# Optimization experiments

Hardware: AMD Instinct MI355X
Metric: run time of the kernel (lower is better)

## Reference

```python
import jax, jax.numpy as jnp
import numpy as np

B, L, E, H = 1, 4096, 1024, 16
D = E // H
EPS = 1e-6


def setup_inputs() -> dict:
    key = jax.random.key(0)
    k1, k2, k3 = jax.random.split(key, 3)
    # fan-in scaled init to keep activations sane
    x = jax.random.normal(k1, (B, L, E), dtype=jnp.float32)
    qkv_w = jax.random.normal(k2, (E, 3 * E), dtype=jnp.float32) / np.sqrt(E)
    qkv_b = jnp.zeros((3 * E,), dtype=jnp.float32)
    out_w = jax.random.normal(k3, (E, E), dtype=jnp.float32) / np.sqrt(E)
    out_b = jnp.zeros((E,), dtype=jnp.float32)
    return {"x": x, "qkv_w": qkv_w, "qkv_b": qkv_b, "out_w": out_w, "out_b": out_b}


def reference(x, qkv_w, qkv_b, out_w, out_b):
    b, l, e = x.shape
    qkv = x @ qkv_w + qkv_b                      # (B, L, 3E)
    q, k, v = jnp.split(qkv, 3, axis=-1)
    # (B, L, E) -> (B, H, L, D)
    q = q.reshape(b, l, H, D).transpose(0, 2, 1, 3)
    k = k.reshape(b, l, H, D).transpose(0, 2, 1, 3)
    v = v.reshape(b, l, H, D).transpose(0, 2, 1, 3)
    q_prime = jax.nn.elu(q) + 1.0
    k_prime = jax.nn.elu(k) + 1.0
    # cumulative sum of per-position outer products k'_l v_l^T : (B,H,L,D,D)
    kv_prod = jnp.einsum('bhld,bhle->bhlde', k_prime, v)
    kv_cumsum = jnp.cumsum(kv_prod, axis=2)
    context = jnp.einsum('bhld,bhlde->bhle', q_prime, kv_cumsum)  # (B,H,L,D)
    k_cumsum = jnp.cumsum(k_prime, axis=2)                        # (B,H,L,D)
    norm = jnp.einsum('bhld,bhld->bhl', q_prime, k_cumsum)        # (B,H,L)
    output = context / (norm[..., None] + EPS)
    output = output.transpose(0, 2, 1, 3).reshape(b, l, e)
    return output @ out_w + out_b
```

## Files before the change

kernel.cpp:

```cpp
#include <hip/hip_runtime.h>
#include <cstddef>
#include <cstdint>

#define L_SEQ 4096
#define EMB   1024
#define NH    16
#define HD    64
#define N3    3072
#define CHUNK 64
#define NCHUNK 64
#define EPS 1e-6f

typedef __attribute__((ext_vector_type(8))) short   bf16x8;
typedef __attribute__((ext_vector_type(4))) short   bf16x4;
typedef __attribute__((ext_vector_type(4))) float   floatx4;

#define AS1 __attribute__((address_space(1)))
#define AS3 __attribute__((address_space(3)))

__device__ __forceinline__ void gload_lds16(const void* g, void* l) {
    __builtin_amdgcn_global_load_lds((AS1 const unsigned int*)g,
                                     (AS3 unsigned int*)l, 16, 0, 0);
}

__device__ __forceinline__ short f2bf(float f) {
    union { float f; unsigned u; } a; a.f = f;
    unsigned r = a.u + 0x7fffu + ((a.u >> 16) & 1u);
    return (short)(r >> 16);
}
__device__ __forceinline__ float bf2f(short s) {
    union { unsigned u; float f; } a; a.u = ((unsigned)(unsigned short)s) << 16;
    return a.f;
}

__device__ __forceinline__ void transpose_tile(const float* __restrict__ W,
                                               short* __restrict__ WT,
                                               int K, int N, int bx, int by,
                                               float (*t)[65], int tid)
{
    const int r  = tid >> 4;
    const int c4 = (tid & 15) << 2;
#pragma unroll
    for (int s = 0; s < 4; ++s) {
        const int k = r + s * 16;
        const floatx4 v = *(const floatx4*)&W[(size_t)(by * 64 + k) * N + bx * 64 + c4];
        t[k][c4 + 0] = v[0]; t[k][c4 + 1] = v[1];
        t[k][c4 + 2] = v[2]; t[k][c4 + 3] = v[3];
    }
    __syncthreads();
#pragma unroll
    for (int s = 0; s < 4; ++s) {
        const int n = r + s * 16;
        bf16x4 o;
        o[0] = f2bf(t[c4 + 0][n]); o[1] = f2bf(t[c4 + 1][n]);
        o[2] = f2bf(t[c4 + 2][n]); o[3] = f2bf(t[c4 + 3][n]);
        *(bf16x4*)&WT[(size_t)(bx * 64 + n) * K + by * 64 + c4] = o;
    }
}

__global__ __launch_bounds__(256)
void prep(const float* __restrict__ x, short* __restrict__ xb,
          const float* __restrict__ qkv_w, short* __restrict__ qwt,
          const float* __restrict__ out_w, short* __restrict__ owt)
{
    __shared__ float t[64][65];
    const int b = blockIdx.x;
    const int tid = threadIdx.x;
    if (b < 2048) {
        const int i = b * 256 + tid;
        const floatx4 a = *(const floatx4*)(x + (size_t)i * 8);
        const floatx4 c = *(const floatx4*)(x + (size_t)i * 8 + 4);
        bf16x8 o;
        o[0] = f2bf(a[0]); o[1] = f2bf(a[1]); o[2] = f2bf(a[2]); o[3] = f2bf(a[3]);
        o[4] = f2bf(c[0]); o[5] = f2bf(c[1]); o[6] = f2bf(c[2]); o[7] = f2bf(c[3]);
        *(bf16x8*)(xb + (size_t)i * 8) = o;
    } else if (b < 2048 + 768) {
        const int u = b - 2048;
        transpose_tile(qkv_w, qwt, EMB, N3, u % 48, u / 48, t, tid);
    } else {
        const int u = b - 2816;
        transpose_tile(out_w, owt, EMB, EMB, u & 15, u >> 4, t, tid);
    }
}

#define CST 136

__global__ __launch_bounds__(256)
void mfma_gemm_qkv(const short* __restrict__ A, const short* __restrict__ BT,
                   const float* __restrict__ bias,
                   short* __restrict__ OQ, short* __restrict__ OK,
                   short* __restrict__ OV, int N, int K)
{
    __shared__ __align__(16) short smem[128 * CST];
    short* pan[4] = { smem, smem + 4096, smem + 8192, smem + 12288 };
    const int tid  = threadIdx.x;
    const int lane = tid & 63;
    const int wave = tid >> 6;
    const int wm = (wave >> 1) * 64;
    const int wn = (wave & 1) * 64;
    const int bx = blockIdx.x;
    const int by = blockIdx.y;
    const int frow = lane & 15;
    const int quad = lane >> 4;
    const int fko  = quad << 3;

    const short* Ab = A  + (size_t)(by * 128) * K;
    const short* Bb = BT + (size_t)(bx * 128) * K;

    floatx4 acc[4][4] = {};

    for (int k0 = 0; k0 < K; k0 += 64) {
#pragma unroll
        for (int p = 0; p < 2; ++p) {
            const int kp = k0 + p * 32;
#pragma unroll
            for (int q = 0; q < 2; ++q) {
                const int ia = q * 256 + tid;
                const int row = ia >> 2;
                const int kc  = (ia & 3) << 3;
                gload_lds16(Ab + (size_t)row * K + kp + kc, &pan[p * 2 + 0][ia << 3]);
                gload_lds16(Bb + (size_t)row * K + kp + kc, &pan[p * 2 + 1][ia << 3]);
            }
        }
        __syncthreads();
#pragma unroll
        for (int p = 0; p < 2; ++p) {
            bf16x8 af[4], bfv[4];
#pragma unroll
            for (int mi = 0; mi < 4; ++mi)
                af[mi] = *(const bf16x8*)&pan[p * 2 + 0][(wm + mi * 16 + frow) * 32 + fko];
#pragma unroll
            for (int ni = 0; ni < 4; ++ni)
                bfv[ni] = *(const bf16x8*)&pan[p * 2 + 1][(wn + ni * 16 + frow) * 32 + fko];
#pragma unroll
            for (int mi = 0; mi < 4; ++mi)
#pragma unroll
                for (int ni = 0; ni < 4; ++ni)
                    acc[mi][ni] = __builtin_amdgcn_mfma_f32_16x16x32_bf16(
                        af[mi], bfv[ni], acc[mi][ni], 0, 0, 0);
        }
        __syncthreads();
    }

    const int rq = quad << 2;
#pragma unroll
    for (int ni = 0; ni < 4; ++ni) {
        const int n = bx * 128 + wn + ni * 16 + frow;
        const float bv = bias[n];
        const bool do_elu = (n >> 10) < 2;
#pragma unroll
        for (int mi = 0; mi < 4; ++mi)
#pragma unroll
            for (int r = 0; r < 4; ++r) {
                float v = acc[mi][ni][r] + bv;
                if (do_elu) v = (v > 0.f) ? (v + 1.f) : __expf(v);
                smem[(wm + mi * 16 + rq + r) * CST + wn + ni * 16 + frow] = f2bf(v);
            }
    }
    __syncthreads();
#pragma unroll
    for (int t = 0; t < 8; ++t) {
        const int idx = t * 256 + tid;
        const int mm = idx >> 4;
        const int c8 = (idx & 15) << 3;
        const bf16x8 val = *(const bf16x8*)&smem[mm * CST + c8];
        const int n0 = bx * 128 + c8;
        const int rsel = n0 >> 10;
        const int h  = (n0 & 1023) >> 6;
        const int d  = n0 & 63;
        short* base = (rsel == 0) ? OQ : (rsel == 1 ? OK : OV);
        *(bf16x8*)&base[((size_t)(h * L_SEQ + by * 128 + mm)) * HD + d] = val;
    }
}

__global__ __launch_bounds__(256)
void mfma_gemm_out(const short* __restrict__ A, const short* __restrict__ BT,
                   const float* __restrict__ bias, float* __restrict__ OF,
                   int N, int K)
{
    __shared__ __align__(16) short smem[12288];
    short* pan[4] = { smem, smem + 2048, smem + 6144, smem + 8192 };
    const int tid  = threadIdx.x;
    const int lane = tid & 63;
    const int wave = tid >> 6;
    const int wm = (wave >> 1) * 32;
    const int wn = (wave & 1) * 64;
    const int bx = blockIdx.x;
    const int by = blockIdx.y;
    const int frow = lane & 15;
    const int quad = lane >> 4;
    const int fko  = quad << 3;

    const short* Ab = A  + (size_t)(by * 64) * K;
    const short* Bb = BT + (size_t)(bx * 128) * K;

    floatx4 acc[2][4] = {};

    for (int k0 = 0; k0 < K; k0 += 64) {
#pragma unroll
        for (int p = 0; p < 2; ++p) {
            const int kp = k0 + p * 32;
            {
                const int row = tid >> 2;
                const int kc  = (tid & 3) << 3;
                gload_lds16(Ab + (size_t)row * K + kp + kc, &pan[p * 2 + 0][tid << 3]);
            }
#pragma unroll
            for (int q = 0; q < 2; ++q) {
                const int ib = q * 256 + tid;
                const int row = ib >> 2;
                const int kc  = (ib & 3) << 3;
                gload_lds16(Bb + (size_t)row * K + kp + kc, &pan[p * 2 + 1][ib << 3]);
            }
        }
        __syncthreads();
#pragma unroll
        for (int p = 0; p < 2; ++p) {
            bf16x8 af[2], bfv[4];
#pragma unroll
            for (int mi = 0; mi < 2; ++mi)
                af[mi] = *(const bf16x8*)&pan[p * 2 + 0][(wm + mi * 16 + frow) * 32 + fko];
#pragma unroll
            for (int ni = 0; ni < 4; ++ni)
                bfv[ni] = *(const bf16x8*)&pan[p * 2 + 1][(wn + ni * 16 + frow) * 32 + fko];
#pragma unroll
            for (int mi = 0; mi < 2; ++mi)
#pragma unroll
                for (int ni = 0; ni < 4; ++ni)
                    acc[mi][ni] = __builtin_amdgcn_mfma_f32_16x16x32_bf16(
                        af[mi], bfv[ni], acc[mi][ni], 0, 0, 0);
        }
        __syncthreads();
    }

    const int rq = quad << 2;
#pragma unroll
    for (int ni = 0; ni < 4; ++ni) {
        const int n = bx * 128 + wn + ni * 16 + frow;
        const float bv = bias[n];
#pragma unroll
        for (int mi = 0; mi < 2; ++mi)
#pragma unroll
            for (int r = 0; r < 4; ++r) {
                const int m = by * 64 + wm + mi * 16 + rq + r;
                OF[(size_t)m * N + n] = acc[mi][ni][r] + bv;
            }
    }
}

#define SP 72

__global__ __launch_bounds__(256, 4)
void chunk_state(const short* __restrict__ Kb, const short* __restrict__ Vb,
                 short* __restrict__ ScTb, float* __restrict__ zc)
{
    __shared__ __align__(16) short Vt[64 * SP];
    __shared__ __align__(16) short Kt[64 * SP];
    const int c = blockIdx.x, h = blockIdx.y;
    const int tid = threadIdx.x, lane = tid & 63, wave = tid >> 6;
    const int frow = lane & 15;
    const int quad = lane >> 4;
    const int fko  = quad << 3;
    const int wm   = wave << 4;
    const short* Kg = Kb + ((size_t)h * L_SEQ + (size_t)c * CHUNK) * HD;
    const short* Vg = Vb + ((size_t)h * L_SEQ + (size_t)c * CHUNK) * HD;

#pragma unroll
    for (int q = 0; q < 2; ++q) {
        const int idx = q * 256 + tid;
        const int l = idx >> 3, c8 = (idx & 7) << 3;
        const bf16x8 vv = *(const bf16x8*)&Vg[l * 64 + c8];
        const bf16x8 kk = *(const bf16x8*)&Kg[l * 64 + c8];
#pragma unroll
        for (int j = 0; j < 8; ++j) {
            Vt[(c8 + j) * SP + l] = vv[j];
            Kt[(c8 + j) * SP + l] = kk[j];
        }
    }
    __syncthreads();

    const bf16x8 af0 = *(const bf16x8*)&Vt[(wm + frow) * SP + fko];
    const bf16x8 af1 = *(const bf16x8*)&Vt[(wm + frow) * SP + 32 + fko];

    floatx4 acc[4] = {};
#pragma unroll
    for (int n = 0; n < 4; ++n) {
        const bf16x8 kf0 = *(const bf16x8*)&Kt[(n * 16 + frow) * SP + fko];
        const bf16x8 kf1 = *(const bf16x8*)&Kt[(n * 16 + frow) * SP + 32 + fko];
        acc[n] = __builtin_amdgcn_mfma_f32_16x16x32_bf16(af0, kf0, acc[n], 0, 0, 0);
        acc[n] = __builtin_amdgcn_mfma_f32_16x16x32_bf16(af1, kf1, acc[n], 0, 0, 0);
    }

    short* Sout = ScTb + (size_t)(h * NCHUNK + c) * 4096;
#pragma unroll
    for (int n = 0; n < 4; ++n)
#pragma unroll
        for (int r = 0; r < 4; ++r) {
            const int e = wm + quad * 4 + r;
            const int d = n * 16 + frow;
            Sout[e * 64 + d] = f2bf(acc[n][r]);
        }

    if (wave == 0) {
        bf16x8 ones;
#pragma unroll
        for (int j = 0; j < 8; ++j) ones[j] = (short)0x3F80;
        floatx4 zacc[4] = {};
#pragma unroll
        for (int n = 0; n < 4; ++n) {
            const bf16x8 kf0 = *(const bf16x8*)&Kt[(n * 16 + frow) * SP + fko];
            const bf16x8 kf1 = *(const bf16x8*)&Kt[(n * 16 + frow) * SP + 32 + fko];
            zacc[n] = __builtin_amdgcn_mfma_f32_16x16x32_bf16(ones, kf0, zacc[n], 0, 0, 0);
            zacc[n] = __builtin_amdgcn_mfma_f32_16x16x32_bf16(ones, kf1, zacc[n], 0, 0, 0);
        }
        if (quad == 0) {
#pragma unroll
            for (int n = 0; n < 4; ++n)
                zc[(size_t)(h * NCHUNK + c) * 64 + n * 16 + frow] = zacc[n][0];
        }
    }
}

__global__ __launch_bounds__(256)
void prefix_scan(const short* __restrict__ ScTb, const float* __restrict__ zc,
                 short* __restrict__ S0b)
{
    const int g = blockIdx.x * 256 + threadIdx.x;
    const int h  = g >> 12;
    const int ed = g & 4095;
    const int e  = ed >> 6;
    const int d  = ed & 63;
    const short* src = ScTb + (size_t)h * NCHUNK * 4096 + ed;
    float run = 0.f;
    for (int cb = 0; cb < NCHUNK; cb += 8) {
        short v[8];
#pragma unroll
        for (int u = 0; u < 8; ++u) v[u] = src[(size_t)(cb + u) * 4096];
#pragma unroll
        for (int u = 0; u < 8; ++u) {
            S0b[((size_t)((h * NCHUNK + cb + u) * 65 + e)) * 64 + d] = f2bf(run);
            run += bf2f(v[u]);
        }
    }
    if (g < NH * HD) {
        const int h2 = g >> 6, d2 = g & 63;
        float rz = 0.f;
        for (int cb = 0; cb < NCHUNK; cb += 8) {
            float w[8];
#pragma unroll
            for (int u = 0; u < 8; ++u)
                w[u] = zc[((size_t)(h2 * NCHUNK + cb + u)) * HD + d2];
#pragma unroll
            for (int u = 0; u < 8; ++u) {
                S0b[((size_t)((h2 * NCHUNK + cb + u) * 65 + 64)) * 64 + d2] = f2bf(rz);
                rz += w[u];
            }
        }
    }
}

__global__ __launch_bounds__(256)
void chunk_attn(const short* __restrict__ Qb, const short* __restrict__ Kb,
                const short* __restrict__ Vb, const short* __restrict__ S0b,
                short* __restrict__ attn)
{
    __shared__ __align__(16) short Vs[65 * SP];
    __shared__ __align__(16) short As[64 * SP];
    const int c = blockIdx.x, h = blockIdx.y;
    const int tid = threadIdx.x, lane = tid & 63, wave = tid >> 6;
    const size_t rb = ((size_t)h * L_SEQ + (size_t)c * CHUNK) * HD;
    const short* Qg = Qb + rb;
    const short* Kg = Kb + rb;
    const short* Vg = Vb + rb;
    const short* Sg = S0b + (size_t)(h * NCHUNK + c) * 65 * 64;

#pragma unroll
    for (int q = 0; q < 2; ++q) {
        const int idx = q * 256 + tid;
        const int row = idx >> 3, c8 = (idx & 7) << 3;
        const bf16x8 vv = *(const bf16x8*)&Vg[row * 64 + c8];
#pragma unroll
        for (int j = 0; j < 8; ++j) Vs[(c8 + j) * SP + row] = vv[j];
    }
    if (tid < 64) Vs[64 * SP + tid] = (short)0x3F80;
    __syncthreads();

    const int frow = lane & 15;
    const int quad = lane >> 4;
    const int fko  = quad << 3;
    const int wm   = wave << 4;

    const bf16x8 qf0 = *(const bf16x8*)&Qg[(wm + frow) * 64 + fko];
    const bf16x8 qf1 = *(const bf16x8*)&Qg[(wm + frow) * 64 + 32 + fko];

    floatx4 sacc[4] = {};
#pragma unroll
    for (int n = 0; n < 4; ++n) {
        const bf16x8 kf0 = *(const bf16x8*)&Kg[(n * 16 + frow) * 64 + fko];
        const bf16x8 kf1 = *(const bf16x8*)&Kg[(n * 16 + frow) * 64 + 32 + fko];
        sacc[n] = __builtin_amdgcn_mfma_f32_16x16x32_bf16(qf0, kf0, sacc[n], 0, 0, 0);
        sacc[n] = __builtin_amdgcn_mfma_f32_16x16x32_bf16(qf1, kf1, sacc[n], 0, 0, 0);
    }
#pragma unroll
    for (int n = 0; n < 4; ++n)
#pragma unroll
        for (int r = 0; r < 4; ++r) {
            const int i = wm + quad * 4 + r;
            const int j = n * 16 + frow;
            As[i * SP + j] = (j <= i) ? f2bf(sacc[n][r]) : (short)0;
        }
    const bf16x8 af0 = *(const bf16x8*)&As[(wm + frow) * SP + fko];
    const bf16x8 af1 = *(const bf16x8*)&As[(wm + frow) * SP + 32 + fko];

    floatx4 oacc[5] = {};
#pragma unroll
    for (int n = 0; n < 4; ++n) {
        const bf16x8 vf0 = *(const bf16x8*)&Vs[(n * 16 + frow) * SP + fko];
        const bf16x8 vf1 = *(const bf16x8*)&Vs[(n * 16 + frow) * SP + 32 + fko];
        oacc[n] = __builtin_amdgcn_mfma_f32_16x16x32_bf16(af0, vf0, oacc[n], 0, 0, 0);
        oacc[n] = __builtin_amdgcn_mfma_f32_16x16x32_bf16(af1, vf1, oacc[n], 0, 0, 0);
        const bf16x8 sf0 = *(const bf16x8*)&Sg[(n * 16 + frow) * 64 + fko];
        const bf16x8 sf1 = *(const bf16x8*)&Sg[(n * 16 + frow) * 64 + 32 + fko];
        oacc[n] = __builtin_amdgcn_mfma_f32_16x16x32_bf16(qf0, sf0, oacc[n], 0, 0, 0);
        oacc[n] = __builtin_amdgcn_mfma_f32_16x16x32_bf16(qf1, sf1, oacc[n], 0, 0, 0);
    }
    {
        const bf16x8 vf0 = *(const bf16x8*)&Vs[64 * SP + fko];
        const bf16x8 vf1 = *(const bf16x8*)&Vs[64 * SP + 32 + fko];
        oacc[4] = __builtin_amdgcn_mfma_f32_16x16x32_bf16(af0, vf0, oacc[4], 0, 0, 0);
        oacc[4] = __builtin_amdgcn_mfma_f32_16x16x32_bf16(af1, vf1, oacc[4], 0, 0, 0);
        const bf16x8 sf0 = *(const bf16x8*)&Sg[64 * 64 + fko];
        const bf16x8 sf1 = *(const bf16x8*)&Sg[64 * 64 + 32 + fko];
        oacc[4] = __builtin_amdgcn_mfma_f32_16x16x32_bf16(qf0, sf0, oacc[4], 0, 0, 0);
        oacc[4] = __builtin_amdgcn_mfma_f32_16x16x32_bf16(qf1, sf1, oacc[4], 0, 0, 0);
    }
#pragma unroll
    for (int r = 0; r < 4; ++r) {
        const float norm = __shfl(oacc[4][r], lane & 48) + EPS;
        const float inv = 1.f / norm;
        const int i = wm + quad * 4 + r;
#pragma unroll
        for (int n = 0; n < 4; ++n)
            As[i * SP + n * 16 + frow] = f2bf(oacc[n][r] * inv);
    }
    __syncthreads();
#pragma unroll
    for (int t = 0; t < 2; ++t) {
        const int idx = t * 256 + tid;
        const int row = idx >> 3, c8 = (idx & 7) << 3;
        *(bf16x8*)&attn[(size_t)(c * CHUNK + row) * EMB + h * HD + c8] =
            *(const bf16x8*)&As[row * SP + c8];
    }
}

extern "C" void kernel_launch(void* const* d_in, const int* in_sizes, int n_in,
                              void* d_out, int out_size, void* d_ws, size_t ws_size,
                              hipStream_t stream)
{
    const float* x     = (const float*)d_in[0];
    const float* qkv_w = (const float*)d_in[1];
    const float* qkv_b = (const float*)d_in[2];
    const float* out_w = (const float*)d_in[3];
    const float* out_b = (const float*)d_in[4];
    float* out = (float*)d_out;

    short* ws    = (short*)d_ws;
    short* Qb    = ws;
    short* Kb    = Qb + 4194304;
    short* Vb    = Kb + 4194304;
    short* xb    = Vb + 4194304;
    short* qwt   = xb + 4194304;
    short* owt   = qwt + 3145728;
    short* attnb = owt + 1048576;
    short* ScTb  = attnb + 4194304;
    short* S0b   = ScTb + 4194304;
    float* zc    = (float*)(S0b + 4259840);

    prep<<<dim3(3072), 256, 0, stream>>>(x, xb, qkv_w, qwt, out_w, owt);
    mfma_gemm_qkv<<<dim3(N3 / 128, L_SEQ / 128), 256, 0, stream>>>(
        xb, qwt, qkv_b, Qb, Kb, Vb, N3, EMB);
    chunk_state<<<dim3(NCHUNK, NH), 256, 0, stream>>>(Kb, Vb, ScTb, zc);
    prefix_scan<<<dim3((NH * 4096) / 256), 256, 0, stream>>>(ScTb, zc, S0b);
    chunk_attn<<<dim3(NCHUNK, NH), 256, 0, stream>>>(Qb, Kb, Vb, S0b, attnb);
    mfma_gemm_out<<<dim3(EMB / 128, L_SEQ / 64), 256, 0, stream>>>(
        attnb, owt, out_b, out, EMB, EMB);
}
```

Baseline: 164.9 us.

## Fuse chunk prefix scan into chunk_state via last-block atomic counter

Removes the separate prefix_scan launch by having the last-finishing chunk_state block of each head, detected with an atomic per-head counter reset in prep, perform the cross-chunk prefix sum of KV states and key sums. The scan now uses 16-element vectorised bf16 loads and stores per thread. This removes a kernel launch and a dependency gap, but concentrates the scan for each head onto a single block, reducing its parallelism. The occupancy hint on chunk_state is also dropped.

```diff
diff --git a/kernel.cpp b/kernel.cpp
--- a/kernel.cpp
+++ b/kernel.cpp
@@ -61,11 +61,13 @@
 __global__ __launch_bounds__(256)
 void prep(const float* __restrict__ x, short* __restrict__ xb,
           const float* __restrict__ qkv_w, short* __restrict__ qwt,
-          const float* __restrict__ out_w, short* __restrict__ owt)
+          const float* __restrict__ out_w, short* __restrict__ owt,
+          int* __restrict__ cnt)
 {
     __shared__ float t[64][65];
     const int b = blockIdx.x;
     const int tid = threadIdx.x;
+    if (b == 0 && tid < NH) cnt[tid] = 0;
     if (b < 2048) {
         const int i = b * 256 + tid;
         const floatx4 a = *(const floatx4*)(x + (size_t)i * 8);
@@ -250,12 +252,14 @@
 
 #define SP 72
 
-__global__ __launch_bounds__(256, 4)
+__global__ __launch_bounds__(256)
 void chunk_state(const short* __restrict__ Kb, const short* __restrict__ Vb,
-                 short* __restrict__ ScTb, float* __restrict__ zc)
+                 short* __restrict__ ScTb, float* __restrict__ zc,
+                 short* __restrict__ S0b, int* __restrict__ cnt)
 {
     __shared__ __align__(16) short Vt[64 * SP];
     __shared__ __align__(16) short Kt[64 * SP];
+    __shared__ int isLast;
     const int c = blockIdx.x, h = blockIdx.y;
     const int tid = threadIdx.x, lane = tid & 63, wave = tid >> 6;
     const int frow = lane & 15;
@@ -319,40 +323,58 @@
                 zc[(size_t)(h * NCHUNK + c) * 64 + n * 16 + frow] = zacc[n][0];
         }
     }
-}
-
-__global__ __launch_bounds__(256)
-void prefix_scan(const short* __restrict__ ScTb, const float* __restrict__ zc,
-                 short* __restrict__ S0b)
-{
-    const int g = blockIdx.x * 256 + threadIdx.x;
-    const int h  = g >> 12;
-    const int ed = g & 4095;
-    const int e  = ed >> 6;
-    const int d  = ed & 63;
-    const short* src = ScTb + (size_t)h * NCHUNK * 4096 + ed;
-    float run = 0.f;
-    for (int cb = 0; cb < NCHUNK; cb += 8) {
-        short v[8];
-#pragma unroll
-        for (int u = 0; u < 8; ++u) v[u] = src[(size_t)(cb + u) * 4096];
-#pragma unroll
-        for (int u = 0; u < 8; ++u) {
-            S0b[((size_t)((h * NCHUNK + cb + u) * 65 + e)) * 64 + d] = f2bf(run);
-            run += bf2f(v[u]);
-        }
-    }
-    if (g < NH * HD) {
-        const int h2 = g >> 6, d2 = g & 63;
+
+    __threadfence();
+    __syncthreads();
+    if (tid == 0) {
+        const int prev = atomicAdd(&cnt[h], 1);
+        isLast = (prev == NCHUNK - 1);
+    }
+    __syncthreads();
+    if (!isLast) return;
+    __threadfence();
+
+    {
+        const int ed0 = tid * 16;
+        const int e  = ed0 >> 6;
+        const int d0 = ed0 & 63;
+        const short* src = ScTb + (size_t)h * NCHUNK * 4096 + ed0;
+        float s[16];
+#pragma unroll
+        for (int j = 0; j < 16; ++j) s[j] = 0.f;
+        for (int cb = 0; cb < NCHUNK; cb += 4) {
+            bf16x8 v0[4], v1[4];
+#pragma unroll
+            for (int u = 0; u < 4; ++u) {
+                v0[u] = *(const bf16x8*)(src + (size_t)(cb + u) * 4096);
+                v1[u] = *(const bf16x8*)(src + (size_t)(cb + u) * 4096 + 8);
+            }
+#pragma unroll
+            for (int u = 0; u < 4; ++u) {
+                bf16x8 o0, o1;
+#pragma unroll
+                for (int j = 0; j < 8; ++j) { o0[j] = f2bf(s[j]); o1[j] = f2bf(s[8 + j]); }
+                short* dst = S0b + ((size_t)((h * NCHUNK + cb + u) * 65 + e)) * 64 + d0;
+                *(bf16x8*)dst       = o0;
+                *(bf16x8*)(dst + 8) = o1;
+#pragma unroll
+                for (int j = 0; j < 8; ++j) {
+                    s[j]     += bf2f(v0[u][j]);
+                    s[8 + j] += bf2f(v1[u][j]);
+                }
+            }
+        }
+    }
+    if (tid < 64) {
         float rz = 0.f;
+        const float* zp = zc + (size_t)h * NCHUNK * 64 + tid;
         for (int cb = 0; cb < NCHUNK; cb += 8) {
             float w[8];
 #pragma unroll
-            for (int u = 0; u < 8; ++u)
-                w[u] = zc[((size_t)(h2 * NCHUNK + cb + u)) * HD + d2];
+            for (int u = 0; u < 8; ++u) w[u] = zp[(size_t)(cb + u) * 64];
 #pragma unroll
             for (int u = 0; u < 8; ++u) {
-                S0b[((size_t)((h2 * NCHUNK + cb + u) * 65 + 64)) * 64 + d2] = f2bf(rz);
+                S0b[((size_t)((h * NCHUNK + cb + u) * 65 + 64)) * 64 + tid] = f2bf(rz);
                 rz += w[u];
             }
         }
@@ -475,12 +497,12 @@
     short* ScTb  = attnb + 4194304;
     short* S0b   = ScTb + 4194304;
     float* zc    = (float*)(S0b + 4259840);
-
-    prep<<<dim3(3072), 256, 0, stream>>>(x, xb, qkv_w, qwt, out_w, owt);
+    int*   cnt   = (int*)(zc + 65536);
+
+    prep<<<dim3(3072), 256, 0, stream>>>(x, xb, qkv_w, qwt, out_w, owt, cnt);
     mfma_gemm_qkv<<<dim3(N3 / 128, L_SEQ / 128), 256, 0, stream>>>(
         xb, qwt, qkv_b, Qb, Kb, Vb, N3, EMB);
-    chunk_state<<<dim3(NCHUNK, NH), 256, 0, stream>>>(Kb, Vb, ScTb, zc);
-    prefix_scan<<<dim3((NH * 4096) / 256), 256, 0, stream>>>(ScTb, zc, S0b);
+    chunk_state<<<dim3(NCHUNK, NH), 256, 0, stream>>>(Kb, Vb, ScTb, zc, S0b, cnt);
     chunk_attn<<<dim3(NCHUNK, NH), 256, 0, stream>>>(Qb, Kb, Vb, S0b, attnb);
     mfma_gemm_out<<<dim3(EMB / 128, L_SEQ / 64), 256, 0, stream>>>(
         attnb, owt, out_b, out, EMB, EMB);
```

Result: slower. 340.5 us (+106.5%).
